# Kernel optimization log

Measured on AMD Instinct MI355X. Metric: run time of the kernel, lower is better.

## Reference

```python
import jax, jax.numpy as jnp
import numpy as np
from jax import lax
from jax.scipy.special import logsumexp

LAM = 10.0
MAX_ITER = 50
CONST = 1e-06


def setup_inputs() -> dict:
    key = jax.random.key(0)
    k1, k2 = jax.random.split(key)
    X = jax.random.normal(k1, (8192, 256), dtype=jnp.float32)
    Y = jax.random.normal(k2, (8192, 256), dtype=jnp.float32)
    return {"X": X, "Y": Y}


def _cost_matrix(X, Y):
    # ||x_i - y_j|| via the gemm identity; same math as sqrt(sum((x-y)^2)+const)
    x2 = jnp.sum(X * X, axis=1, keepdims=True)          # [n,1]
    y2 = jnp.sum(Y * Y, axis=1, keepdims=True)          # [m,1]
    sq = x2 + y2.T - 2.0 * (X @ Y.T)                     # [n,m]
    return jnp.sqrt(jnp.maximum(sq, 0.0) + CONST)


def reference(X, Y):
    n, m = X.shape[0], Y.shape[0]
    C = _cost_matrix(X, Y)                               # [n,m]
    log_a = -jnp.log(jnp.asarray(n, C.dtype))            # log(1/n)
    log_b = -jnp.log(jnp.asarray(m, C.dtype))            # log(1/m)
    f0 = jnp.zeros((n, 1), C.dtype)
    g0 = jnp.zeros((m, 1), C.dtype)

    def body(carry, _):
        f, g = carry
        K = (-C + f + g.T) / LAM
        f = LAM * (log_a - logsumexp(K, axis=1, keepdims=True)) + f
        K = (-C + f + g.T) / LAM
        g = LAM * (log_b - logsumexp(K, axis=0, keepdims=True).T) + g
        return (f, g), None

    (f, g), _ = lax.scan(body, (f0, g0), None, length=MAX_ITER)
    pi = jnp.exp((-C + f + g.T) / LAM)
    cost = jnp.sum(pi * C)
    return cost, pi
```

## Files before the change

kernel.cpp:

```cpp
#include <hip/hip_runtime.h>
#include <cstdint>
#include <cstddef>

static constexpr int Nn = 8192;
static constexpr int Mm = 8192;
static constexpr int Kd = 256;
static constexpr float LAM_F   = 10.0f;
static constexpr float INV_N_F = 1.0f / 8192.0f;

typedef _Float16 h16;
typedef _Float16 h16x4 __attribute__((ext_vector_type(4)));
typedef _Float16 f16x8 __attribute__((ext_vector_type(8)));
typedef float    f32x16 __attribute__((ext_vector_type(16)));

__device__ __forceinline__ float dec1_fp8(uint32_t b) {
  uint32_t e = (b >> 3) & 15u, m = b & 7u;
  float n = __uint_as_float(((e + 120u) << 23) | (m << 20));
  float s = (float)m * 0.001953125f;
  return e ? n : s;
}
__device__ __forceinline__ void cvt4_fp8(uint32_t w, float* o) {
#if __has_builtin(__builtin_amdgcn_cvt_pk_f32_fp8)
  auto lo = __builtin_amdgcn_cvt_pk_f32_fp8(w, false);
  auto hi = __builtin_amdgcn_cvt_pk_f32_fp8(w, true);
  o[0] = lo[0]; o[1] = lo[1]; o[2] = hi[0]; o[3] = hi[1];
#else
  o[0] = dec1_fp8(w & 255u); o[1] = dec1_fp8((w >> 8) & 255u);
  o[2] = dec1_fp8((w >> 16) & 255u); o[3] = dec1_fp8(w >> 24);
#endif
}
__device__ __forceinline__ uint8_t enc1_fp8(float x) {
#if __has_builtin(__builtin_amdgcn_cvt_pk_fp8_f32)
  return (uint8_t)(__builtin_amdgcn_cvt_pk_fp8_f32(x, x, 0, false) & 0xff);
#else
  uint32_t b = __float_as_uint(x);
  int e = (int)((b >> 23) & 255) - 127;
  uint32_t m = b & 0x7fffffu;
  if (e < -9) return 0;
  if (e >= -6) {
    uint32_t keep = m >> 20, rest = m & 0xfffffu;
    if (rest > 0x80000u || (rest == 0x80000u && (keep & 1u))) keep++;
    return (uint8_t)(((uint32_t)(e + 7) << 3) + keep);
  }
  return (uint8_t)(int)(x * 512.0f + 0.5f);
#endif
}

__device__ __forceinline__ void load8(const float* p, float* o) {
#pragma unroll
  for (int i = 0; i < 8; ++i) o[i] = p[i];
}
__device__ __forceinline__ void store4e(float* p, float a, float b, float c, float d) {
  p[0] = a; p[1] = b; p[2] = c; p[3] = d;
}

__global__ __launch_bounds__(256) void setup_kernel(
    const float* __restrict__ X, const float* __restrict__ Y,
    float* __restrict__ x2, float* __restrict__ y2,
    float* __restrict__ u, float* __restrict__ cost,
    h16* __restrict__ Xh, h16* __restrict__ Yh) {
  const int gid  = blockIdx.x * blockDim.x + threadIdx.x;
  const int wid  = gid >> 6;
  const int lane = threadIdx.x & 63;
  const bool isX = wid < Nn;
  const int row  = isX ? wid : wid - Nn;
  const float4* rp = (const float4*)((isX ? X : Y) + (size_t)row * Kd);
  float4 q = rp[lane];
  h16x4 hq; hq[0] = (h16)q.x; hq[1] = (h16)q.y; hq[2] = (h16)q.z; hq[3] = (h16)q.w;
  *(h16x4*)((isX ? Xh : Yh) + (size_t)row * Kd + lane * 4) = hq;
  float s = q.x*q.x + q.y*q.y + q.z*q.z + q.w*q.w;
#pragma unroll
  for (int o = 32; o > 0; o >>= 1) s += __shfl_down(s, o);
  if (lane == 0) { if (isX) x2[row] = s; else y2[row] = s; }
  if (gid < Mm) u[gid] = 1.0f;
  if (gid == 0) cost[0] = 0.0f;
}

__global__ __launch_bounds__(256) void build_e8_mfma(
    const h16* __restrict__ Xh, const h16* __restrict__ Yh,
    const float* __restrict__ x2, const float* __restrict__ y2,
    uint8_t* __restrict__ E8) {
  __shared__ h16 smem[16384];
  __shared__ float x2s[128], y2s[128];
  const int tid = threadIdx.x;
  const int i0 = blockIdx.y * 128, j0 = blockIdx.x * 128;
  if (tid < 128) x2s[tid] = x2[i0 + tid];
  else           y2s[tid - 128] = y2[j0 + tid - 128];

  f32x16 acc[2][2];
#pragma unroll
  for (int a = 0; a < 2; ++a)
#pragma unroll
    for (int b = 0; b < 2; ++b)
#pragma unroll
      for (int r = 0; r < 16; ++r) acc[a][b][r] = 0.0f;

  const int w = tid >> 6, lane = tid & 63;
  const int mt0 = (w >> 1) * 2, nt0 = (w & 1) * 2;

  for (int kc = 0; kc < 4; ++kc) {
    __syncthreads();
#pragma unroll
    for (int p = 0; p < 4; ++p) {
      const int c  = p * 256 + tid;
      const int r  = c >> 3, k8 = c & 7;
      const int mt = r >> 5, m = r & 31, s = k8 >> 1, hf = k8 & 1;
      const int dst = ((mt * 4 + s) * 64 + m + 32 * hf) * 8;
      *(uint4*)(smem + dst)        = *(const uint4*)(Xh + (size_t)(i0 + r) * Kd + kc * 64 + k8 * 8);
      *(uint4*)(smem + 8192 + dst) = *(const uint4*)(Yh + (size_t)(j0 + r) * Kd + kc * 64 + k8 * 8);
    }
    __syncthreads();
#pragma unroll
    for (int s = 0; s < 4; ++s) {
      f16x8 a0 = *(const f16x8*)(smem + (((mt0    ) * 4 + s) * 64 + lane) * 8);
      f16x8 a1 = *(const f16x8*)(smem + (((mt0 + 1) * 4 + s) * 64 + lane) * 8);
      f16x8 b0 = *(const f16x8*)(smem + 8192 + (((nt0    ) * 4 + s) * 64 + lane) * 8);
      f16x8 b1 = *(const f16x8*)(smem + 8192 + (((nt0 + 1) * 4 + s) * 64 + lane) * 8);
      acc[0][0] = __builtin_amdgcn_mfma_f32_32x32x16_f16(a0, b0, acc[0][0], 0, 0, 0);
      acc[0][1] = __builtin_amdgcn_mfma_f32_32x32x16_f16(a0, b1, acc[0][1], 0, 0, 0);
      acc[1][0] = __builtin_amdgcn_mfma_f32_32x32x16_f16(a1, b0, acc[1][0], 0, 0, 0);
      acc[1][1] = __builtin_amdgcn_mfma_f32_32x32x16_f16(a1, b1, acc[1][1], 0, 0, 0);
    }
  }

  __syncthreads();
  uint8_t* tile8 = (uint8_t*)smem;
  const int mq = (w >> 1) * 64, nq = (w & 1) * 64;
#pragma unroll
  for (int ti = 0; ti < 2; ++ti)
#pragma unroll
    for (int tj = 0; tj < 2; ++tj) {
      const int colb = nq + tj * 32 + (lane & 31);
      const float yv = y2s[colb];
#pragma unroll
      for (int r = 0; r < 16; ++r) {
        const int rowb = mq + ti * 32 + (r & 3) + 8 * (r >> 2) + 4 * (lane >> 5);
        float sq = x2s[rowb] + yv - 2.0f * acc[ti][tj][r];
        float cc = sqrtf(fmaxf(sq, 0.0f) + 1e-6f);
        tile8[rowb * 128 + colb] = enc1_fp8(__expf(-0.1f * cc));
      }
    }
  __syncthreads();
#pragma unroll
  for (int p = 0; p < 4; ++p) {
    const int c = p * 256 + tid;
    const int r = c >> 3, k = c & 7;
    *(uint4*)(E8 + (size_t)(i0 + r) * Mm + j0 + k * 16) = *(const uint4*)(tile8 + r * 128 + k * 16);
  }
}

__global__ __launch_bounds__(256) void row_pass8_kernel(
    const uint8_t* __restrict__ E8, const float* __restrict__ u, float* __restrict__ v) {
  const int wid  = (blockIdx.x * blockDim.x + threadIdx.x) >> 6;
  const int lane = threadIdx.x & 63;
  const int r0   = wid * 2;
  const uint8_t* row = E8 + (size_t)r0 * Mm;
  float s0 = 0.0f, s1 = 0.0f;
#pragma unroll 1
  for (int g = 0; g < 8; g += 2) {
    const int ja = (g * 64 + lane) * 16;
    const int jb = ((g + 1) * 64 + lane) * 16;
    uint4 qa0 = *(const uint4*)(row + ja);
    uint4 qa1 = *(const uint4*)(row + (size_t)Mm + ja);
    uint4 qb0 = *(const uint4*)(row + jb);
    uint4 qb1 = *(const uint4*)(row + (size_t)Mm + jb);
    float4 uu[8];
#pragma unroll
    for (int i = 0; i < 4; ++i) uu[i]     = *(const float4*)(u + ja + i * 4);
#pragma unroll
    for (int i = 0; i < 4; ++i) uu[4 + i] = *(const float4*)(u + jb + i * 4);
    const uint32_t wa0[4] = {qa0.x, qa0.y, qa0.z, qa0.w};
    const uint32_t wa1[4] = {qa1.x, qa1.y, qa1.z, qa1.w};
    const uint32_t wb0[4] = {qb0.x, qb0.y, qb0.z, qb0.w};
    const uint32_t wb1[4] = {qb1.x, qb1.y, qb1.z, qb1.w};
#pragma unroll
    for (int d = 0; d < 4; ++d) {
      float f0[4], f1[4];
      const float* up = (const float*)&uu[d];
      cvt4_fp8(wa0[d], f0); cvt4_fp8(wa1[d], f1);
#pragma unroll
      for (int i = 0; i < 4; ++i) { s0 = fmaf(f0[i], up[i], s0); s1 = fmaf(f1[i], up[i], s1); }
    }
#pragma unroll
    for (int d = 0; d < 4; ++d) {
      float f0[4], f1[4];
      const float* up = (const float*)&uu[4 + d];
      cvt4_fp8(wb0[d], f0); cvt4_fp8(wb1[d], f1);
#pragma unroll
      for (int i = 0; i < 4; ++i) { s0 = fmaf(f0[i], up[i], s0); s1 = fmaf(f1[i], up[i], s1); }
    }
  }
#pragma unroll
  for (int o = 32; o > 0; o >>= 1) { s0 += __shfl_down(s0, o); s1 += __shfl_down(s1, o); }
  if (lane == 0) *(float2*)(v + r0) = make_float2(INV_N_F / s0, INV_N_F / s1);
}

__global__ __launch_bounds__(256) void col_pass8_kernel(
    const uint8_t* __restrict__ E8, const float* __restrict__ v, float* __restrict__ part) {
  const int c0 = blockIdx.x * 4096 + threadIdx.x * 16;
  const int r0 = blockIdx.y * 64;
  const uint8_t* base = E8 + (size_t)r0 * Mm + c0;
  float acc[16] = {};
#pragma unroll 1
  for (int rb = 0; rb < 64; rb += 8) {
    uint4 q[8];
#pragma unroll
    for (int r = 0; r < 8; ++r) q[r] = *(const uint4*)(base + (size_t)(rb + r) * Mm);
#pragma unroll
    for (int r = 0; r < 8; ++r) {
      const float vr = v[r0 + rb + r];
      const uint32_t wd[4] = {q[r].x, q[r].y, q[r].z, q[r].w};
#pragma unroll
      for (int d = 0; d < 4; ++d) {
        float f[4]; cvt4_fp8(wd[d], f);
#pragma unroll
        for (int i = 0; i < 4; ++i) acc[d * 4 + i] = fmaf(f[i], vr, acc[d * 4 + i]);
      }
    }
  }
  float* dst = part + (size_t)blockIdx.y * Mm + c0;
#pragma unroll
  for (int d = 0; d < 4; ++d)
    *((float4*)dst + d) = make_float4(acc[d*4], acc[d*4+1], acc[d*4+2], acc[d*4+3]);
}

__global__ __launch_bounds__(256) void combine_kernel(
    const float* __restrict__ part, float* __restrict__ u) {
  const int j = blockIdx.x * blockDim.x + threadIdx.x;
  float t = 0.0f;
#pragma unroll 8
  for (int c = 0; c < 128; ++c) t += part[(size_t)c * Mm + j];
  u[j] = INV_N_F / t;
}

__global__ __launch_bounds__(256) void final_mfma(
    const h16* __restrict__ Xh, const h16* __restrict__ Yh,
    const float* __restrict__ x2, const float* __restrict__ y2,
    const float* __restrict__ v, const float* __restrict__ u,
    float* __restrict__ pi, float* __restrict__ cost) {
  __shared__ h16 smem[16384];
  __shared__ float x2s[128], y2s[128], vs[128], us[128];
  const int tid = threadIdx.x;
  const int i0 = blockIdx.y * 128, j0 = blockIdx.x * 128;
  if (tid < 128) { x2s[tid] = x2[i0 + tid]; vs[tid] = v[i0 + tid]; }
  else           { y2s[tid - 128] = y2[j0 + tid - 128]; us[tid - 128] = u[j0 + tid - 128]; }

  f32x16 acc[2][2];
#pragma unroll
  for (int a = 0; a < 2; ++a)
#pragma unroll
    for (int b = 0; b < 2; ++b)
#pragma unroll
      for (int r = 0; r < 16; ++r) acc[a][b][r] = 0.0f;

  const int w = tid >> 6, lane = tid & 63;
  const int mt0 = (w >> 1) * 2, nt0 = (w & 1) * 2;

  for (int kc = 0; kc < 4; ++kc) {
    __syncthreads();
#pragma unroll
    for (int p = 0; p < 4; ++p) {
      const int c  = p * 256 + tid;
      const int r  = c >> 3, k8 = c & 7;
      const int mt = r >> 5, m = r & 31, s = k8 >> 1, hf = k8 & 1;
      const int dst = ((mt * 4 + s) * 64 + m + 32 * hf) * 8;
      *(uint4*)(smem + dst)        = *(const uint4*)(Xh + (size_t)(i0 + r) * Kd + kc * 64 + k8 * 8);
      *(uint4*)(smem + 8192 + dst) = *(const uint4*)(Yh + (size_t)(j0 + r) * Kd + kc * 64 + k8 * 8);
    }
    __syncthreads();
#pragma unroll
    for (int s = 0; s < 4; ++s) {
      f16x8 a0 = *(const f16x8*)(smem + (((mt0    ) * 4 + s) * 64 + lane) * 8);
      f16x8 a1 = *(const f16x8*)(smem + (((mt0 + 1) * 4 + s) * 64 + lane) * 8);
      f16x8 b0 = *(const f16x8*)(smem + 8192 + (((nt0    ) * 4 + s) * 64 + lane) * 8);
      f16x8 b1 = *(const f16x8*)(smem + 8192 + (((nt0 + 1) * 4 + s) * 64 + lane) * 8);
      acc[0][0] = __builtin_amdgcn_mfma_f32_32x32x16_f16(a0, b0, acc[0][0], 0, 0, 0);
      acc[0][1] = __builtin_amdgcn_mfma_f32_32x32x16_f16(a0, b1, acc[0][1], 0, 0, 0);
      acc[1][0] = __builtin_amdgcn_mfma_f32_32x32x16_f16(a1, b0, acc[1][0], 0, 0, 0);
      acc[1][1] = __builtin_amdgcn_mfma_f32_32x32x16_f16(a1, b1, acc[1][1], 0, 0, 0);
    }
  }

  const int mq = (w >> 1) * 64, nq = (w & 1) * 64;
  float csum = 0.0f;
#pragma unroll
  for (int ti = 0; ti < 2; ++ti)
#pragma unroll
    for (int tj = 0; tj < 2; ++tj) {
      const int colb = nq + tj * 32 + (lane & 31);
      const float yv = y2s[colb], uu = us[colb];
#pragma unroll
      for (int r = 0; r < 16; ++r) {
        const int rowb = mq + ti * 32 + (r & 3) + 8 * (r >> 2) + 4 * (lane >> 5);
        float sq = x2s[rowb] + yv - 2.0f * acc[ti][tj][r];
        float cc = sqrtf(fmaxf(sq, 0.0f) + 1e-6f);
        float p  = vs[rowb] * __expf(-0.1f * cc) * uu;
        pi[(size_t)(i0 + rowb) * Mm + j0 + colb] = p;
        csum = fmaf(p, cc, csum);
      }
    }
#pragma unroll
  for (int o = 32; o > 0; o >>= 1) csum += __shfl_down(csum, o);
  if (lane == 0) atomicAdd(cost, csum);
}

template <typename ET>
__global__ __launch_bounds__(256) void build_e_f32(
    const float* __restrict__ X, const float* __restrict__ Y,
    const float* __restrict__ x2, const float* __restrict__ y2,
    ET* __restrict__ E) {
  __shared__ float As[64][66];
  __shared__ float Bs[64][66];
  const int tid = threadIdx.x;
  const int tx = tid & 15;
  const int ty = tid >> 4;
  const int i0 = blockIdx.y * 64;
  const int j0 = blockIdx.x * 64;
  float acc[4][4] = {};
  for (int k0 = 0; k0 < Kd; k0 += 64) {
    __syncthreads();
#pragma unroll
    for (int rep = 0; rep < 16; ++rep) {
      const int e = rep * 256 + tid;
      const int k = e & 63, i = e >> 6;
      As[k][i] = X[(size_t)(i0 + i) * Kd + k0 + k];
      Bs[k][i] = Y[(size_t)(j0 + i) * Kd + k0 + k];
    }
    __syncthreads();
    for (int k = 0; k < 64; ++k) {
      float a0 = As[k][ty*4+0], a1 = As[k][ty*4+1], a2 = As[k][ty*4+2], a3 = As[k][ty*4+3];
      float b0 = Bs[k][tx*4+0], b1 = Bs[k][tx*4+1], b2 = Bs[k][tx*4+2], b3 = Bs[k][tx*4+3];
      acc[0][0] += a0*b0; acc[0][1] += a0*b1; acc[0][2] += a0*b2; acc[0][3] += a0*b3;
      acc[1][0] += a1*b0; acc[1][1] += a1*b1; acc[1][2] += a1*b2; acc[1][3] += a1*b3;
      acc[2][0] += a2*b0; acc[2][1] += a2*b1; acc[2][2] += a2*b2; acc[2][3] += a2*b3;
      acc[3][0] += a3*b0; acc[3][1] += a3*b1; acc[3][2] += a3*b2; acc[3][3] += a3*b3;
    }
  }
  float xx[4], yy[4];
#pragma unroll
  for (int d = 0; d < 4; ++d) { xx[d] = x2[i0 + ty*4 + d]; yy[d] = y2[j0 + tx*4 + d]; }
#pragma unroll
  for (int di = 0; di < 4; ++di) {
    float e4[4];
#pragma unroll
    for (int dj = 0; dj < 4; ++dj) {
      float sq = xx[di] + yy[dj] - 2.0f * acc[di][dj];
      float c  = sqrtf(fmaxf(sq, 0.0f) + 1e-6f);
      e4[dj] = __expf(-c * 0.1f);
    }
    store4e(&E[(size_t)(i0 + ty*4 + di) * Mm + j0 + tx*4], e4[0], e4[1], e4[2], e4[3]);
  }
}

template <typename ET>
__global__ __launch_bounds__(256) void row_pass_kernel(
    const ET* __restrict__ E, const float* __restrict__ u, float* __restrict__ v) {
  const int wid  = (blockIdx.x * blockDim.x + threadIdx.x) >> 6;
  const int lane = threadIdx.x & 63;
  const ET* row = E + (size_t)wid * Mm;
  float s = 0.0f;
#pragma unroll 4
  for (int g = 0; g < 16; ++g) {
    const int j8 = (g * 64 + lane) * 8;
    float ev[8]; load8(row + j8, ev);
    const float4 u0 = *(const float4*)(u + j8);
    const float4 u1 = *(const float4*)(u + j8 + 4);
    s += ev[0]*u0.x + ev[1]*u0.y + ev[2]*u0.z + ev[3]*u0.w;
    s += ev[4]*u1.x + ev[5]*u1.y + ev[6]*u1.z + ev[7]*u1.w;
  }
#pragma unroll
  for (int o = 32; o > 0; o >>= 1) s += __shfl_down(s, o);
  if (lane == 0) v[wid] = INV_N_F / s;
}

template <typename ET>
__global__ __launch_bounds__(256) void col_pass_kernel(
    const ET* __restrict__ E, const float* __restrict__ v, float* __restrict__ part) {
  const int c0 = blockIdx.x * 2048 + threadIdx.x * 8;
  const int r0 = blockIdx.y * 64;
  float acc[8] = {};
#pragma unroll 4
  for (int r = r0; r < r0 + 64; ++r) {
    const float vr = v[r];
    float ev[8]; load8(E + (size_t)r * Mm + c0, ev);
#pragma unroll
    for (int c = 0; c < 8; ++c) acc[c] += ev[c] * vr;
  }
  float* dst = part + (size_t)blockIdx.y * Mm + c0;
  *(float4*)dst       = make_float4(acc[0], acc[1], acc[2], acc[3]);
  *((float4*)dst + 1) = make_float4(acc[4], acc[5], acc[6], acc[7]);
}

template <typename ET>
__global__ __launch_bounds__(256) void final_pass_kernel(
    const ET* E, const float* __restrict__ v, const float* __restrict__ u,
    float* pi, float* cost) {
  const int wid  = (blockIdx.x * blockDim.x + threadIdx.x) >> 6;
  const int lane = threadIdx.x & 63;
  const ET* row = E + (size_t)wid * Mm;
  float* prow = pi + (size_t)wid * Mm;
  const float vi = v[wid];
  float csum = 0.0f;
  for (int g = 0; g < 16; ++g) {
    const int j8 = (g * 64 + lane) * 8;
    float ev[8]; load8(row + j8, ev);
#pragma unroll
    for (int c = 0; c < 8; ++c) {
      const float uu  = u[j8 + c];
      const float p   = vi * ev[c] * uu;
      const float Cij = -LAM_F * __logf(ev[c]);
      prow[j8 + c] = p;
      csum += p * Cij;
    }
  }
#pragma unroll
  for (int o = 32; o > 0; o >>= 1) csum += __shfl_down(csum, o);
  if (lane == 0) atomicAdd(cost, csum);
}

extern "C" void kernel_launch(void* const* d_in, const int* in_sizes, int n_in,
                              void* d_out, int out_size, void* d_ws, size_t ws_size,
                              hipStream_t stream) {
  const float* X = (const float*)d_in[0];
  const float* Y = (const float*)d_in[1];
  float* out  = (float*)d_out;
  float* cost = out;
  float* pi   = out + 1;

  char*  ws   = (char*)d_ws;
  float* x2   = (float*)ws;
  float* y2   = x2 + Nn;
  float* u    = y2 + Mm;
  float* v    = u + Mm;
  float* part = v + Nn;
  h16*   XhW  = (h16*)(part + (size_t)128 * Mm);
  h16*   YhW  = XhW + (size_t)Nn * Kd;
  const size_t pre_bytes = (size_t)((char*)(YhW + (size_t)Mm * Kd) - ws);
  const size_t e_off = (pre_bytes + 255) & ~(size_t)255;
  const bool fast = ws_size >= e_off + (size_t)Nn * Mm + 256;

  h16* Xh = fast ? XhW : (h16*)(((uintptr_t)pi + 15) & ~(uintptr_t)15);
  h16* Yh = Xh + (size_t)Nn * Kd;

  setup_kernel<<<4096, 256, 0, stream>>>(X, Y, x2, y2, u, cost, Xh, Yh);

  if (fast) {
    uint8_t* E8 = (uint8_t*)ws + e_off;
    build_e8_mfma<<<dim3(64, 64), 256, 0, stream>>>(Xh, Yh, x2, y2, E8);
    for (int it = 0; it < 50; ++it) {
      row_pass8_kernel<<<1024, 256, 0, stream>>>(E8, u, v);
      col_pass8_kernel<<<dim3(2, 128), 256, 0, stream>>>(E8, v, part);
      combine_kernel<<<32, 256, 0, stream>>>(part, u);
    }
    final_mfma<<<dim3(64, 64), 256, 0, stream>>>(Xh, Yh, x2, y2, v, u, pi, cost);
  } else {
    float* E = pi;
    build_e_f32<float><<<dim3(128, 128), 256, 0, stream>>>(X, Y, x2, y2, E);
    for (int it = 0; it < 50; ++it) {
      row_pass_kernel<float><<<2048, 256, 0, stream>>>(E, u, v);
      col_pass_kernel<float><<<dim3(4, 128), 256, 0, stream>>>(E, v, part);
      combine_kernel<<<32, 256, 0, stream>>>(part, u);
    }
    final_pass_kernel<float><<<2048, 256, 0, stream>>>(E, v, u, pi, cost);
  }
}
```

Measured before the change: 2.220 ms.

## Swizzle LDS fragments, stage u in shared memory, coalesce pi stores

XOR-swizzles the shared-memory slots for the fp16 MFMA operand tiles in both the build and final kernels to avoid LDS bank conflicts. The row pass now loads the whole u vector into shared memory once per block instead of reading it from global memory per wave. The final kernel stages the pi tile in a 64KB shared buffer and writes it back with 16-byte coalesced stores, where it previously did scattered 4-byte stores. The larger LDS footprint may lower occupancy of the final kernel and adds extra barriers.

```diff
diff --git a/kernel.cpp b/kernel.cpp
--- a/kernel.cpp
+++ b/kernel.cpp
@@ -44,6 +44,10 @@
   }
   return (uint8_t)(int)(x * 512.0f + 0.5f);
 #endif
+}
+
+__device__ __forceinline__ int frag_slot(int t, int s, int l) {
+  return (t * 4 + s) * 64 + (l & 32) + ((l & 31) ^ (2 * s + (l >> 5)));
 }
 
 __device__ __forceinline__ void load8(const float* p, float* o) {
@@ -105,17 +109,17 @@
       const int c  = p * 256 + tid;
       const int r  = c >> 3, k8 = c & 7;
       const int mt = r >> 5, m = r & 31, s = k8 >> 1, hf = k8 & 1;
-      const int dst = ((mt * 4 + s) * 64 + m + 32 * hf) * 8;
-      *(uint4*)(smem + dst)        = *(const uint4*)(Xh + (size_t)(i0 + r) * Kd + kc * 64 + k8 * 8);
-      *(uint4*)(smem + 8192 + dst) = *(const uint4*)(Yh + (size_t)(j0 + r) * Kd + kc * 64 + k8 * 8);
+      const int slot = (mt * 4 + s) * 64 + hf * 32 + (m ^ k8);
+      *(uint4*)(smem + slot * 8)        = *(const uint4*)(Xh + (size_t)(i0 + r) * Kd + kc * 64 + k8 * 8);
+      *(uint4*)(smem + 8192 + slot * 8) = *(const uint4*)(Yh + (size_t)(j0 + r) * Kd + kc * 64 + k8 * 8);
     }
     __syncthreads();
 #pragma unroll
     for (int s = 0; s < 4; ++s) {
-      f16x8 a0 = *(const f16x8*)(smem + (((mt0    ) * 4 + s) * 64 + lane) * 8);
-      f16x8 a1 = *(const f16x8*)(smem + (((mt0 + 1) * 4 + s) * 64 + lane) * 8);
-      f16x8 b0 = *(const f16x8*)(smem + 8192 + (((nt0    ) * 4 + s) * 64 + lane) * 8);
-      f16x8 b1 = *(const f16x8*)(smem + 8192 + (((nt0 + 1) * 4 + s) * 64 + lane) * 8);
+      f16x8 a0 = *(const f16x8*)(smem + frag_slot(mt0,     s, lane) * 8);
+      f16x8 a1 = *(const f16x8*)(smem + frag_slot(mt0 + 1, s, lane) * 8);
+      f16x8 b0 = *(const f16x8*)(smem + 8192 + frag_slot(nt0,     s, lane) * 8);
+      f16x8 b1 = *(const f16x8*)(smem + 8192 + frag_slot(nt0 + 1, s, lane) * 8);
       acc[0][0] = __builtin_amdgcn_mfma_f32_32x32x16_f16(a0, b0, acc[0][0], 0, 0, 0);
       acc[0][1] = __builtin_amdgcn_mfma_f32_32x32x16_f16(a0, b1, acc[0][1], 0, 0, 0);
       acc[1][0] = __builtin_amdgcn_mfma_f32_32x32x16_f16(a1, b0, acc[1][0], 0, 0, 0);
@@ -151,6 +155,13 @@
 
 __global__ __launch_bounds__(256) void row_pass8_kernel(
     const uint8_t* __restrict__ E8, const float* __restrict__ u, float* __restrict__ v) {
+  __shared__ float us[8192];
+#pragma unroll
+  for (int i = 0; i < 8; ++i) {
+    const int o = (i * 256 + threadIdx.x) * 4;
+    *(float4*)(us + o) = *(const float4*)(u + o);
+  }
+  __syncthreads();
   const int wid  = (blockIdx.x * blockDim.x + threadIdx.x) >> 6;
   const int lane = threadIdx.x & 63;
   const int r0   = wid * 2;
@@ -164,11 +175,6 @@
     uint4 qa1 = *(const uint4*)(row + (size_t)Mm + ja);
     uint4 qb0 = *(const uint4*)(row + jb);
     uint4 qb1 = *(const uint4*)(row + (size_t)Mm + jb);
-    float4 uu[8];
-#pragma unroll
-    for (int i = 0; i < 4; ++i) uu[i]     = *(const float4*)(u + ja + i * 4);
-#pragma unroll
-    for (int i = 0; i < 4; ++i) uu[4 + i] = *(const float4*)(u + jb + i * 4);
     const uint32_t wa0[4] = {qa0.x, qa0.y, qa0.z, qa0.w};
     const uint32_t wa1[4] = {qa1.x, qa1.y, qa1.z, qa1.w};
     const uint32_t wb0[4] = {qb0.x, qb0.y, qb0.z, qb0.w};
@@ -176,7 +182,8 @@
 #pragma unroll
     for (int d = 0; d < 4; ++d) {
       float f0[4], f1[4];
-      const float* up = (const float*)&uu[d];
+      const float4 uv = *(const float4*)(us + ja + d * 4);
+      const float up[4] = {uv.x, uv.y, uv.z, uv.w};
       cvt4_fp8(wa0[d], f0); cvt4_fp8(wa1[d], f1);
 #pragma unroll
       for (int i = 0; i < 4; ++i) { s0 = fmaf(f0[i], up[i], s0); s1 = fmaf(f1[i], up[i], s1); }
@@ -184,7 +191,8 @@
 #pragma unroll
     for (int d = 0; d < 4; ++d) {
       float f0[4], f1[4];
-      const float* up = (const float*)&uu[4 + d];
+      const float4 uv = *(const float4*)(us + jb + d * 4);
+      const float up[4] = {uv.x, uv.y, uv.z, uv.w};
       cvt4_fp8(wb0[d], f0); cvt4_fp8(wb1[d], f1);
 #pragma unroll
       for (int i = 0; i < 4; ++i) { s0 = fmaf(f0[i], up[i], s0); s1 = fmaf(f1[i], up[i], s1); }
@@ -238,7 +246,9 @@
     const float* __restrict__ x2, const float* __restrict__ y2,
     const float* __restrict__ v, const float* __restrict__ u,
     float* __restrict__ pi, float* __restrict__ cost) {
-  __shared__ h16 smem[16384];
+  __shared__ __align__(16) unsigned char smemraw[65536];
+  h16*   smem = (h16*)smemraw;
+  float* tile = (float*)smemraw;
   __shared__ float x2s[128], y2s[128], vs[128], us[128];
   const int tid = threadIdx.x;
   const int i0 = blockIdx.y * 128, j0 = blockIdx.x * 128;
@@ -263,17 +273,17 @@
       const int c  = p * 256 + tid;
       const int r  = c >> 3, k8 = c & 7;
       const int mt = r >> 5, m = r & 31, s = k8 >> 1, hf = k8 & 1;
-      const int dst = ((mt * 4 + s) * 64 + m + 32 * hf) * 8;
-      *(uint4*)(smem + dst)        = *(const uint4*)(Xh + (size_t)(i0 + r) * Kd + kc * 64 + k8 * 8);
-      *(uint4*)(smem + 8192 + dst) = *(const uint4*)(Yh + (size_t)(j0 + r) * Kd + kc * 64 + k8 * 8);
+      const int slot = (mt * 4 + s) * 64 + hf * 32 + (m ^ k8);
+      *(uint4*)(smem + slot * 8)        = *(const uint4*)(Xh + (size_t)(i0 + r) * Kd + kc * 64 + k8 * 8);
+      *(uint4*)(smem + 8192 + slot * 8) = *(const uint4*)(Yh + (size_t)(j0 + r) * Kd + kc * 64 + k8 * 8);
     }
     __syncthreads();
 #pragma unroll
     for (int s = 0; s < 4; ++s) {
-      f16x8 a0 = *(const f16x8*)(smem + (((mt0    ) * 4 + s) * 64 + lane) * 8);
-      f16x8 a1 = *(const f16x8*)(smem + (((mt0 + 1) * 4 + s) * 64 + lane) * 8);
-      f16x8 b0 = *(const f16x8*)(smem + 8192 + (((nt0    ) * 4 + s) * 64 + lane) * 8);
-      f16x8 b1 = *(const f16x8*)(smem + 8192 + (((nt0 + 1) * 4 + s) * 64 + lane) * 8);
+      f16x8 a0 = *(const f16x8*)(smem + frag_slot(mt0,     s, lane) * 8);
+      f16x8 a1 = *(const f16x8*)(smem + frag_slot(mt0 + 1, s, lane) * 8);
+      f16x8 b0 = *(const f16x8*)(smem + 8192 + frag_slot(nt0,     s, lane) * 8);
+      f16x8 b1 = *(const f16x8*)(smem + 8192 + frag_slot(nt0 + 1, s, lane) * 8);
       acc[0][0] = __builtin_amdgcn_mfma_f32_32x32x16_f16(a0, b0, acc[0][0], 0, 0, 0);
       acc[0][1] = __builtin_amdgcn_mfma_f32_32x32x16_f16(a0, b1, acc[0][1], 0, 0, 0);
       acc[1][0] = __builtin_amdgcn_mfma_f32_32x32x16_f16(a1, b0, acc[1][0], 0, 0, 0);
@@ -281,6 +291,7 @@
     }
   }
 
+  __syncthreads();
   const int mq = (w >> 1) * 64, nq = (w & 1) * 64;
   float csum = 0.0f;
 #pragma unroll
@@ -295,10 +306,17 @@
         float sq = x2s[rowb] + yv - 2.0f * acc[ti][tj][r];
         float cc = sqrtf(fmaxf(sq, 0.0f) + 1e-6f);
         float p  = vs[rowb] * __expf(-0.1f * cc) * uu;
-        pi[(size_t)(i0 + rowb) * Mm + j0 + colb] = p;
+        tile[rowb * 128 + colb] = p;
         csum = fmaf(p, cc, csum);
       }
     }
+  __syncthreads();
+#pragma unroll
+  for (int it2 = 0; it2 < 16; ++it2) {
+    const int c = it2 * 256 + tid;
+    const int r = c >> 5, k = c & 31;
+    *(uint4*)(pi + (size_t)(i0 + r) * Mm + j0 + k * 4) = *(const uint4*)(tile + r * 128 + k * 4);
+  }
 #pragma unroll
   for (int o = 32; o > 0; o >>= 1) csum += __shfl_down(csum, o);
   if (lane == 0) atomicAdd(cost, csum);
```

After: 2.152 ms. 1.03x faster.
